# Optimization experiments

Measured on AMD Instinct MI355X. Metric: run time of the kernel, lower is better.

## Reference

```python
import jax, jax.numpy as jnp
import numpy as np

SEQ, BS, H, D = 2048, 2, 16, 64


def phi(x):
    # ELU(x / d**0.25) + 1
    return jax.nn.elu(x / (x.shape[-1] ** 0.25)) + 1.0


def setup_inputs() -> dict:
    key = jax.random.key(0)
    ks = jax.random.split(key, 5)
    return {
        "query_layer": jax.random.normal(ks[0], (SEQ, BS, H, D), jnp.float32),
        "key_layer": jax.random.normal(ks[1], (SEQ, BS, H, D), jnp.float32),
        "value_layer": jax.random.normal(ks[2], (SEQ, BS, H, D), jnp.float32),
        "attention_mask": jnp.zeros((BS, 1, SEQ, SEQ), dtype=bool),  # unused by forward
        "phi_k": jax.random.normal(ks[3], (1, H, D, 1), jnp.float32) / 10000.0,
        "phi_kv": jax.random.normal(ks[4], (1, H, D, D), jnp.float32) / 10000.0,
    }


def _ntk_attn(q, k, v, sum_phi_k, sum_phi_kv):
    # q,k,v: [bs,h,n,d]; sum_phi_k: [1,h,d,1]; sum_phi_kv: [1,h,d,d]
    d = q.shape[-1]
    nq, nk = q.shape[-2], k.shape[-2]
    kk = jnp.abs(sum_phi_k)
    Z = sum_phi_kv
    phi_q = phi(q)  # [bs,h,nq,d]
    A = jnp.einsum("bhqd,bhkd->bhqk", q, k) / jnp.sqrt(jnp.float32(d))
    max_A = jnp.max(A, axis=-1, keepdims=True)  # [bs,h,nq,1]
    exp_max_A = jnp.exp(max_A)
    A = jnp.exp(A - max_A)
    causal = jnp.tril(jnp.ones((nq, nk), jnp.float32), k=nk - nq)
    A = A * causal  # broadcast over [bs,h]
    D_norm = jnp.sum(A, axis=-1, keepdims=True) + jnp.matmul(phi_q, kk) / exp_max_A
    ctx = (jnp.matmul(A, v) + jnp.matmul(phi_q, Z) / exp_max_A) / D_norm
    return ctx  # [bs,h,nq,d]


def reference(query_layer, key_layer, value_layer, attention_mask, phi_k, phi_kv):
    # inputs are [seq, bs, h, d]; attention_mask is unused (module ignores it)
    q = jnp.transpose(query_layer, (1, 2, 0, 3)).astype(jnp.float32)
    k = jnp.transpose(key_layer, (1, 2, 0, 3)).astype(jnp.float32)
    v = jnp.transpose(value_layer, (1, 2, 0, 3)).astype(jnp.float32)
    ctx = _ntk_attn(q, k, v, phi_k, phi_kv)  # [bs,h,nq,d]
    ctx = jnp.transpose(ctx, (2, 0, 1, 3))  # [nq,bs,h,d]
    nq, bs, h, d = ctx.shape
    return ctx.reshape(nq, bs, h * d).astype(query_layer.dtype)
```

## Files before the change

### kernel.cpp

```cpp
#include <hip/hip_runtime.h>

#define SEQ 2048
#define BSZ 2
#define NHEAD 16
#define NBH (BSZ * NHEAD)
#define HDIM 64
#define QBLK 64
#define KVBLK 64
#define NQT (SEQ / QBLK)
#define ROWSTRIDE (BSZ * NHEAD * HDIM)

typedef __bf16 bf16x8 __attribute__((ext_vector_type(8)));
typedef __bf16 bf16x4 __attribute__((ext_vector_type(4)));
typedef float f32x4 __attribute__((ext_vector_type(4)));

#define AS1 __attribute__((address_space(1)))
#define AS3 __attribute__((address_space(3)))

__global__ __launch_bounds__(256)
void conv_all(const float* __restrict__ Kg, const float* __restrict__ Vg,
              const float* __restrict__ PKVg, __bf16* __restrict__ Kb,
              __bf16* __restrict__ Vt, __bf16* __restrict__ Ztb) {
  __shared__ __bf16 tt[HDIM][72];
  const int b = blockIdx.x;
  const int tid = threadIdx.x;

  if (b < 2048) {
    const int t = b * 256 + tid;
    const int s = t >> 8;
    const int bh = (t >> 3) & 31;
    const int d8 = (t & 7) * 8;
    const float* src = Kg + (size_t)s * ROWSTRIDE + bh * HDIM + d8;
    const float4 a = *(const float4*)src;
    const float4 bb = *(const float4*)(src + 4);
    bf16x8 o = {(__bf16)a.x, (__bf16)a.y, (__bf16)a.z, (__bf16)a.w,
                (__bf16)bb.x, (__bf16)bb.y, (__bf16)bb.z, (__bf16)bb.w};
    const int slot = (d8 >> 3) ^ (s & 7);
    *(bf16x8*)(Kb + ((size_t)bh * SEQ + s) * HDIM + slot * 8) = o;
  } else if (b < 3072) {
    const int t = b - 2048;
    const int kb = t & 31, bh = t >> 5;
    {
      const int r = tid >> 2, c16 = (tid & 3) * 16;
#pragma unroll
      for (int i = 0; i < 4; ++i) {
        const float4 v = *(const float4*)(Vg + (size_t)(kb * 64 + r) * ROWSTRIDE +
                                          bh * HDIM + c16 + 4 * i);
        tt[c16 + 4 * i + 0][r] = (__bf16)v.x;
        tt[c16 + 4 * i + 1][r] = (__bf16)v.y;
        tt[c16 + 4 * i + 2][r] = (__bf16)v.z;
        tt[c16 + 4 * i + 3][r] = (__bf16)v.w;
      }
    }
    __syncthreads();
    {
      const int d = tid >> 2, c2 = (tid & 3) * 2;
#pragma unroll
      for (int k8 = 0; k8 < 2; ++k8) {
        const int s8 = c2 + k8;
        const int pbase = (s8 ^ (d & 7)) * 8;
        __bf16 ov[8];
#pragma unroll
        for (int j = 0; j < 8; ++j) {
          const int p = pbase + j;
          const int P = p >> 5, g = (p >> 3) & 3, jj = p & 7;
          ov[j] = tt[d][32 * P + 16 * (jj >> 2) + 4 * g + (jj & 3)];
        }
        *(bf16x8*)(Vt + (((size_t)bh * 32 + kb) * 64 + d) * 64 + s8 * 8) =
            *(const bf16x8*)ov;
      }
    }
  } else {
    const int t = (b - 3072) * 256 + tid;
    const int lr = t & 15, lg = (t >> 4) & 3, c = (t >> 6) & 1;
    const int dj = (t >> 7) & 3, h = t >> 9;
    __bf16 o[8];
#pragma unroll
    for (int i = 0; i < 8; ++i)
      o[i] = (__bf16)PKVg[((size_t)h * 64 + 32 * c + 8 * lg + i) * 64 + dj * 16 + lr];
    *(bf16x8*)(Ztb + (size_t)t * 8) = *(const bf16x8*)o;
  }
}

__global__ __launch_bounds__(256, 4)
void ntk_attn(const float* __restrict__ Qg, const __bf16* __restrict__ Kb,
              const __bf16* __restrict__ Vt, const float* __restrict__ PKg,
              const __bf16* __restrict__ Ztb, float* __restrict__ Og) {
  __shared__ __bf16 Ks[2][KVBLK * HDIM];
  __shared__ __bf16 Vts[2][KVBLK * HDIM];

  const int tid = threadIdx.x;
  const int w = tid >> 6, l = tid & 63, lr = l & 15, lg = l >> 4;

  const int ord = blockIdx.x;
  const int bh = ord & 31, h = bh & (NHEAD - 1);
  const int v = ord >> 5;
  const int bx = (v < 16) ? v : 47 - v;
  const int q0 = bx * QBLK;
  const int ntile = bx + 1;
  const int headoff = bh * HDIM;
  const __bf16* Kbh = Kb + (size_t)bh * SEQ * HDIM;
  const __bf16* Vbh = Vt + (size_t)bh * SEQ * HDIM;

  auto stage = [&](int kb, int bb) {
    const char* gk = (const char*)Kbh + ((size_t)kb << 13) + (w << 11) + (l << 4);
    const char* gv = (const char*)Vbh + ((size_t)kb << 13) + (w << 11) + (l << 4);
    __bf16* lk = &Ks[bb][w << 10];
    __bf16* lv = &Vts[bb][w << 10];
    __builtin_amdgcn_global_load_lds((const AS1 unsigned*)gk,
                                     (AS3 unsigned*)lk, 16, 0, 0);
    __builtin_amdgcn_global_load_lds((const AS1 unsigned*)(gk + 1024),
                                     (AS3 unsigned*)(lk + 512), 16, 0, 0);
    __builtin_amdgcn_global_load_lds((const AS1 unsigned*)gv,
                                     (AS3 unsigned*)lv, 16, 0, 0);
    __builtin_amdgcn_global_load_lds((const AS1 unsigned*)(gv + 1024),
                                     (AS3 unsigned*)(lv + 512), 16, 0, 0);
  };

  stage(0, 0);

  bf16x8 aq[2], pq[2];
  {
    const float* qp = Qg + (size_t)(q0 + w * 16 + lr) * ROWSTRIDE + headoff + lg * 8;
#pragma unroll
    for (int c = 0; c < 2; ++c) {
      const float4 x0 = *(const float4*)(qp + 32 * c);
      const float4 x1 = *(const float4*)(qp + 32 * c + 4);
      const float f[8] = {x0.x, x0.y, x0.z, x0.w, x1.x, x1.y, x1.z, x1.w};
#pragma unroll
      for (int i = 0; i < 8; ++i) {
        aq[c][i] = (__bf16)(f[i] * 0.18033688011112042f);
        const float xs = f[i] * 0.3535533905932738f;
        pq[c][i] = (__bf16)(xs > 0.f ? xs + 1.f : __expf(xs));
      }
    }
  }

  const f32x4 z4 = {0.f, 0.f, 0.f, 0.f};
  f32x4 oacc[4] = {z4, z4, z4, z4};
  float lsum = 0.f;
  const int qa = q0 + w * 16 + lr;
  const int sw = lr & 7;

  __syncthreads();
  int cur = 0;

  for (int kb = 0; kb < ntile; ++kb) {
    const bool more = (kb + 1 < ntile);
    if (more) stage(kb + 1, cur ^ 1);

    bf16x8 kc[4][2];
#pragma unroll
    for (int nj = 0; nj < 4; ++nj)
#pragma unroll
      for (int c = 0; c < 2; ++c)
        kc[nj][c] = *(const bf16x8*)&Ks[cur][(nj * 16 + lr) * 64 +
                                            (((4 * c + lg) ^ sw) << 3)];
    bf16x8 vv[2][4];
#pragma unroll
    for (int P = 0; P < 2; ++P)
#pragma unroll
      for (int dj = 0; dj < 4; ++dj)
        vv[P][dj] = *(const bf16x8*)&Vts[cur][(dj * 16 + lr) * 64 +
                                             (((4 * P + lg) ^ sw) << 3)];

    f32x4 s4[4];
    __builtin_amdgcn_s_setprio(1);
#pragma unroll
    for (int nj = 0; nj < 4; ++nj) {
      f32x4 acc = z4;
#pragma unroll
      for (int c = 0; c < 2; ++c)
        acc = __builtin_amdgcn_mfma_f32_16x16x32_bf16(kc[nj][c], aq[c], acc, 0, 0, 0);
      s4[nj] = acc;
    }
    __builtin_amdgcn_s_setprio(0);

    bf16x4 p4[4];
    const bool diag = (kb == bx);
    const int kv0 = kb * KVBLK;
#pragma unroll
    for (int nj = 0; nj < 4; ++nj) {
#pragma unroll
      for (int r = 0; r < 4; ++r) {
        float e;
        if (diag) {
          const int kabs = kv0 + 16 * nj + 4 * lg + r;
          e = (kabs <= qa) ? __builtin_amdgcn_exp2f(s4[nj][r]) : 0.f;
        } else {
          e = __builtin_amdgcn_exp2f(s4[nj][r]);
        }
        lsum += e;
        p4[nj][r] = (__bf16)e;
      }
    }

    __builtin_amdgcn_s_setprio(1);
#pragma unroll
    for (int P = 0; P < 2; ++P) {
      const bf16x8 pa = __builtin_shufflevector(p4[2 * P], p4[2 * P + 1],
                                                0, 1, 2, 3, 4, 5, 6, 7);
#pragma unroll
      for (int dj = 0; dj < 4; ++dj)
        oacc[dj] = __builtin_amdgcn_mfma_f32_16x16x32_bf16(pa, vv[P][dj],
                                                           oacc[dj], 0, 0, 0);
    }
    __builtin_amdgcn_s_setprio(0);

    if (more) {
      __syncthreads();
      cur ^= 1;
    }
  }

  float den;
  {
    float pkk = 0.f;
#pragma unroll
    for (int c = 0; c < 2; ++c) {
      const float* kp = PKg + h * HDIM + 32 * c + 8 * lg;
      const float4 a = *(const float4*)kp;
      const float4 b = *(const float4*)(kp + 4);
      const float ka[8] = {a.x, a.y, a.z, a.w, b.x, b.y, b.z, b.w};
#pragma unroll
      for (int i = 0; i < 8; ++i)
        pkk += (float)pq[c][i] * fabsf(ka[i]);
    }
    pkk += __shfl_xor(pkk, 16);
    pkk += __shfl_xor(pkk, 32);
    float s = lsum;
    s += __shfl_xor(s, 16);
    s += __shfl_xor(s, 32);
    den = s + pkk;
  }

  f32x4 zacc[4] = {z4, z4, z4, z4};
  const __bf16* Zf = Ztb + (size_t)h * 4096;
  __builtin_amdgcn_s_setprio(1);
#pragma unroll
  for (int c = 0; c < 2; ++c) {
#pragma unroll
    for (int dj = 0; dj < 4; ++dj) {
      const bf16x8 bz = *(const bf16x8*)(Zf + ((dj * 2 + c) * 64 + l) * 8);
      zacc[dj] = __builtin_amdgcn_mfma_f32_16x16x32_bf16(pq[c], bz, zacc[dj], 0, 0, 0);
    }
  }
  __builtin_amdgcn_s_setprio(0);

#pragma unroll
  for (int r = 0; r < 4; ++r) {
    const float rd = 1.f / __shfl(den, lg * 4 + r);
    float* op = Og + (size_t)(q0 + w * 16 + lg * 4 + r) * ROWSTRIDE + headoff;
#pragma unroll
    for (int dj = 0; dj < 4; ++dj)
      op[dj * 16 + lr] = (oacc[dj][r] + zacc[dj][r]) * rd;
  }
}

extern "C" void kernel_launch(void* const* d_in, const int* in_sizes, int n_in,
                              void* d_out, int out_size, void* d_ws, size_t ws_size,
                              hipStream_t stream) {
  const float* Qg  = (const float*)d_in[0];
  const float* Kg  = (const float*)d_in[1];
  const float* Vg  = (const float*)d_in[2];
  const float* PKg  = (const float*)d_in[4];
  const float* PKVg = (const float*)d_in[5];
  float* Og = (float*)d_out;

  __bf16* Kb  = (__bf16*)d_ws;
  __bf16* Vt  = Kb + (size_t)NBH * SEQ * HDIM;
  __bf16* Ztb = Vt + (size_t)NBH * SEQ * HDIM;

  conv_all<<<dim3(2048 + 1024 + 32), dim3(256), 0, stream>>>(Kg, Vg, PKVg,
                                                             Kb, Vt, Ztb);
  ntk_attn<<<dim3(NQT * NBH), dim3(256), 0, stream>>>(Qg, Kb, Vt, PKg, Ztb, Og);
}
```

Baseline: 46.65 us.

## Process two 64-row query groups per block to reuse staged K/V tiles

```diff
diff --git a/kernel.cpp b/kernel.cpp
--- a/kernel.cpp
+++ b/kernel.cpp
@@ -5,7 +5,7 @@
 #define NHEAD 16
 #define NBH (BSZ * NHEAD)
 #define HDIM 64
-#define QBLK 64
+#define QBLK 128
 #define KVBLK 64
 #define NQT (SEQ / QBLK)
 #define ROWSTRIDE (BSZ * NHEAD * HDIM)
@@ -82,7 +82,7 @@
   }
 }
 
-__global__ __launch_bounds__(256, 4)
+__global__ __launch_bounds__(256, 2)
 void ntk_attn(const float* __restrict__ Qg, const __bf16* __restrict__ Kb,
               const __bf16* __restrict__ Vt, const float* __restrict__ PKg,
               const __bf16* __restrict__ Ztb, float* __restrict__ Og) {
@@ -95,9 +95,10 @@
   const int ord = blockIdx.x;
   const int bh = ord & 31, h = bh & (NHEAD - 1);
   const int v = ord >> 5;
-  const int bx = (v < 16) ? v : 47 - v;
+  const int bx = (v < 8) ? v : 23 - v;
   const int q0 = bx * QBLK;
-  const int ntile = bx + 1;
+  const int ntile = 2 * bx + 2;
+  const int dt0 = 2 * bx;
   const int headoff = bh * HDIM;
   const __bf16* Kbh = Kb + (size_t)bh * SEQ * HDIM;
   const __bf16* Vbh = Vt + (size_t)bh * SEQ * HDIM;
@@ -119,9 +120,11 @@
 
   stage(0, 0);
 
-  bf16x8 aq[2], pq[2];
-  {
-    const float* qp = Qg + (size_t)(q0 + w * 16 + lr) * ROWSTRIDE + headoff + lg * 8;
+  bf16x8 aq[2][2], pq[2][2];
+#pragma unroll
+  for (int g = 0; g < 2; ++g) {
+    const float* qp = Qg + (size_t)(q0 + 64 * g + w * 16 + lr) * ROWSTRIDE +
+                      headoff + lg * 8;
 #pragma unroll
     for (int c = 0; c < 2; ++c) {
       const float4 x0 = *(const float4*)(qp + 32 * c);
@@ -129,17 +132,19 @@
       const float f[8] = {x0.x, x0.y, x0.z, x0.w, x1.x, x1.y, x1.z, x1.w};
 #pragma unroll
       for (int i = 0; i < 8; ++i) {
-        aq[c][i] = (__bf16)(f[i] * 0.18033688011112042f);
+        aq[g][c][i] = (__bf16)(f[i] * 0.18033688011112042f);
         const float xs = f[i] * 0.3535533905932738f;
-        pq[c][i] = (__bf16)(xs > 0.f ? xs + 1.f : __expf(xs));
+        pq[g][c][i] = (__bf16)(xs > 0.f ? xs + 1.f : __expf(xs));
       }
     }
   }
 
   const f32x4 z4 = {0.f, 0.f, 0.f, 0.f};
-  f32x4 oacc[4] = {z4, z4, z4, z4};
-  float lsum = 0.f;
-  const int qa = q0 + w * 16 + lr;
+  f32x4 oacc[2][4] = {{z4, z4, z4, z4}, {z4, z4, z4, z4}};
+  float lsum[2] = {0.f, 0.f};
+  int qa[2];
+  qa[0] = q0 + w * 16 + lr;
+  qa[1] = q0 + 64 + w * 16 + lr;
   const int sw = lr & 7;
 
   __syncthreads();
@@ -164,48 +169,52 @@
         vv[P][dj] = *(const bf16x8*)&Vts[cur][(dj * 16 + lr) * 64 +
                                              (((4 * P + lg) ^ sw) << 3)];
 
-    f32x4 s4[4];
-    __builtin_amdgcn_s_setprio(1);
-#pragma unroll
-    for (int nj = 0; nj < 4; ++nj) {
-      f32x4 acc = z4;
-#pragma unroll
-      for (int c = 0; c < 2; ++c)
-        acc = __builtin_amdgcn_mfma_f32_16x16x32_bf16(kc[nj][c], aq[c], acc, 0, 0, 0);
-      s4[nj] = acc;
-    }
-    __builtin_amdgcn_s_setprio(0);
-
-    bf16x4 p4[4];
-    const bool diag = (kb == bx);
     const int kv0 = kb * KVBLK;
 #pragma unroll
-    for (int nj = 0; nj < 4; ++nj) {
-#pragma unroll
-      for (int r = 0; r < 4; ++r) {
-        float e;
-        if (diag) {
-          const int kabs = kv0 + 16 * nj + 4 * lg + r;
-          e = (kabs <= qa) ? __builtin_amdgcn_exp2f(s4[nj][r]) : 0.f;
-        } else {
-          e = __builtin_amdgcn_exp2f(s4[nj][r]);
+    for (int g = 0; g < 2; ++g) {
+      if (g == 0 && kb > dt0) continue;
+
+      f32x4 s4[4];
+      __builtin_amdgcn_s_setprio(1);
+#pragma unroll
+      for (int nj = 0; nj < 4; ++nj) {
+        f32x4 acc = z4;
+        acc = __builtin_amdgcn_mfma_f32_16x16x32_bf16(kc[nj][0], aq[g][0], acc, 0, 0, 0);
+        acc = __builtin_amdgcn_mfma_f32_16x16x32_bf16(kc[nj][1], aq[g][1], acc, 0, 0, 0);
+        s4[nj] = acc;
+      }
+      __builtin_amdgcn_s_setprio(0);
+
+      bf16x4 p4[4];
+      const bool diag = (kb == dt0 + g);
+#pragma unroll
+      for (int nj = 0; nj < 4; ++nj) {
+#pragma unroll
+        for (int r = 0; r < 4; ++r) {
+          float e;
+          if (diag) {
+            const int kabs = kv0 + 16 * nj + 4 * lg + r;
+            e = (kabs <= qa[g]) ? __builtin_amdgcn_exp2f(s4[nj][r]) : 0.f;
+          } else {
+            e = __builtin_amdgcn_exp2f(s4[nj][r]);
+          }
+          lsum[g] += e;
+          p4[nj][r] = (__bf16)e;
         }
-        lsum += e;
-        p4[nj][r] = (__bf16)e;
-      }
-    }
-
-    __builtin_amdgcn_s_setprio(1);
-#pragma unroll
-    for (int P = 0; P < 2; ++P) {
-      const bf16x8 pa = __builtin_shufflevector(p4[2 * P], p4[2 * P + 1],
-                                                0, 1, 2, 3, 4, 5, 6, 7);
-#pragma unroll
-      for (int dj = 0; dj < 4; ++dj)
-        oacc[dj] = __builtin_amdgcn_mfma_f32_16x16x32_bf16(pa, vv[P][dj],
-                                                           oacc[dj], 0, 0, 0);
-    }
-    __builtin_amdgcn_s_setprio(0);
+      }
+
+      __builtin_amdgcn_s_setprio(1);
+#pragma unroll
+      for (int P = 0; P < 2; ++P) {
+        const bf16x8 pa = __builtin_shufflevector(p4[2 * P], p4[2 * P + 1],
+                                                  0, 1, 2, 3, 4, 5, 6, 7);
+#pragma unroll
+        for (int dj = 0; dj < 4; ++dj)
+          oacc[g][dj] = __builtin_amdgcn_mfma_f32_16x16x32_bf16(pa, vv[P][dj],
+                                                                oacc[g][dj], 0, 0, 0);
+      }
+      __builtin_amdgcn_s_setprio(0);
+    }
 
     if (more) {
       __syncthreads();
@@ -213,47 +222,61 @@
     }
   }
 
-  float den;
+  float ka[16];
   {
-    float pkk = 0.f;
 #pragma unroll
     for (int c = 0; c < 2; ++c) {
       const float* kp = PKg + h * HDIM + 32 * c + 8 * lg;
       const float4 a = *(const float4*)kp;
       const float4 b = *(const float4*)(kp + 4);
-      const float ka[8] = {a.x, a.y, a.z, a.w, b.x, b.y, b.z, b.w};
+      ka[8 * c + 0] = fabsf(a.x); ka[8 * c + 1] = fabsf(a.y);
+      ka[8 * c + 2] = fabsf(a.z); ka[8 * c + 3] = fabsf(a.w);
+      ka[8 * c + 4] = fabsf(b.x); ka[8 * c + 5] = fabsf(b.y);
+      ka[8 * c + 6] = fabsf(b.z); ka[8 * c + 7] = fabsf(b.w);
+    }
+  }
+  bf16x8 bz[2][4];
+  const __bf16* Zf = Ztb + (size_t)h * 4096;
+#pragma unroll
+  for (int c = 0; c < 2; ++c)
+#pragma unroll
+    for (int dj = 0; dj < 4; ++dj)
+      bz[c][dj] = *(const bf16x8*)(Zf + ((dj * 2 + c) * 64 + l) * 8);
+
+#pragma unroll
+  for (int g = 0; g < 2; ++g) {
+    float pkk = 0.f;
+#pragma unroll
+    for (int c = 0; c < 2; ++c)
 #pragma unroll
       for (int i = 0; i < 8; ++i)
-        pkk += (float)pq[c][i] * fabsf(ka[i]);
-    }
+        pkk += (float)pq[g][c][i] * ka[8 * c + i];
     pkk += __shfl_xor(pkk, 16);
     pkk += __shfl_xor(pkk, 32);
-    float s = lsum;
+    float s = lsum[g];
     s += __shfl_xor(s, 16);
     s += __shfl_xor(s, 32);
-    den = s + pkk;
-  }
-
-  f32x4 zacc[4] = {z4, z4, z4, z4};
-  const __bf16* Zf = Ztb + (size_t)h * 4096;
-  __builtin_amdgcn_s_setprio(1);
-#pragma unroll
-  for (int c = 0; c < 2; ++c) {
-#pragma unroll
-    for (int dj = 0; dj < 4; ++dj) {
-      const bf16x8 bz = *(const bf16x8*)(Zf + ((dj * 2 + c) * 64 + l) * 8);
-      zacc[dj] = __builtin_amdgcn_mfma_f32_16x16x32_bf16(pq[c], bz, zacc[dj], 0, 0, 0);
-    }
-  }
-  __builtin_amdgcn_s_setprio(0);
-
-#pragma unroll
-  for (int r = 0; r < 4; ++r) {
-    const float rd = 1.f / __shfl(den, lg * 4 + r);
-    float* op = Og + (size_t)(q0 + w * 16 + lg * 4 + r) * ROWSTRIDE + headoff;
-#pragma unroll
-    for (int dj = 0; dj < 4; ++dj)
-      op[dj * 16 + lr] = (oacc[dj][r] + zacc[dj][r]) * rd;
+    const float den = s + pkk;
+
+    f32x4 zacc[4] = {z4, z4, z4, z4};
+    __builtin_amdgcn_s_setprio(1);
+#pragma unroll
+    for (int c = 0; c < 2; ++c)
+#pragma unroll
+      for (int dj = 0; dj < 4; ++dj)
+        zacc[dj] = __builtin_amdgcn_mfma_f32_16x16x32_bf16(pq[g][c], bz[c][dj],
+                                                           zacc[dj], 0, 0, 0);
+    __builtin_amdgcn_s_setprio(0);
+
+#pragma unroll
+    for (int r = 0; r < 4; ++r) {
+      const float rd = 1.f / __shfl(den, lg * 4 + r);
+      float* op = Og + (size_t)(q0 + 64 * g + w * 16 + lg * 4 + r) * ROWSTRIDE +
+                  headoff;
+#pragma unroll
+      for (int dj = 0; dj < 4; ++dj)
+        op[dj * 16 + lr] = (oacc[g][dj][r] + zacc[dj][r]) * rd;
+    }
   }
 }
 
```

Measured after the change: 46.48 us. About the same (-0.4%).

## Software-pipeline QK^T of next KV tile with PV of current tile

Applied to the files above, without the earlier changes.

```diff
diff --git a/kernel.cpp b/kernel.cpp
--- a/kernel.cpp
+++ b/kernel.cpp
@@ -142,20 +142,32 @@
   const int qa = q0 + w * 16 + lr;
   const int sw = lr & 7;
 
+  bf16x8 kc[4][2];
+  auto read_kc = [&](int bb) {
+#pragma unroll
+    for (int nj = 0; nj < 4; ++nj)
+#pragma unroll
+      for (int c = 0; c < 2; ++c)
+        kc[nj][c] = *(const bf16x8*)&Ks[bb][(nj * 16 + lr) * 64 +
+                                           (((4 * c + lg) ^ sw) << 3)];
+  };
+
+  f32x4 s4[4];
   __syncthreads();
+  read_kc(0);
+  __builtin_amdgcn_s_setprio(1);
+#pragma unroll
+  for (int nj = 0; nj < 4; ++nj) {
+    f32x4 acc = z4;
+    acc = __builtin_amdgcn_mfma_f32_16x16x32_bf16(kc[nj][0], aq[0], acc, 0, 0, 0);
+    acc = __builtin_amdgcn_mfma_f32_16x16x32_bf16(kc[nj][1], aq[1], acc, 0, 0, 0);
+    s4[nj] = acc;
+  }
+  __builtin_amdgcn_s_setprio(0);
+  if (ntile > 1) stage(1, 1);
+
   int cur = 0;
-
   for (int kb = 0; kb < ntile; ++kb) {
-    const bool more = (kb + 1 < ntile);
-    if (more) stage(kb + 1, cur ^ 1);
-
-    bf16x8 kc[4][2];
-#pragma unroll
-    for (int nj = 0; nj < 4; ++nj)
-#pragma unroll
-      for (int c = 0; c < 2; ++c)
-        kc[nj][c] = *(const bf16x8*)&Ks[cur][(nj * 16 + lr) * 64 +
-                                            (((4 * c + lg) ^ sw) << 3)];
     bf16x8 vv[2][4];
 #pragma unroll
     for (int P = 0; P < 2; ++P)
@@ -163,18 +175,6 @@
       for (int dj = 0; dj < 4; ++dj)
         vv[P][dj] = *(const bf16x8*)&Vts[cur][(dj * 16 + lr) * 64 +
                                              (((4 * P + lg) ^ sw) << 3)];
-
-    f32x4 s4[4];
-    __builtin_amdgcn_s_setprio(1);
-#pragma unroll
-    for (int nj = 0; nj < 4; ++nj) {
-      f32x4 acc = z4;
-#pragma unroll
-      for (int c = 0; c < 2; ++c)
-        acc = __builtin_amdgcn_mfma_f32_16x16x32_bf16(kc[nj][c], aq[c], acc, 0, 0, 0);
-      s4[nj] = acc;
-    }
-    __builtin_amdgcn_s_setprio(0);
 
     bf16x4 p4[4];
     const bool diag = (kb == bx);
@@ -195,21 +195,43 @@
       }
     }
 
-    __builtin_amdgcn_s_setprio(1);
-#pragma unroll
-    for (int P = 0; P < 2; ++P) {
-      const bf16x8 pa = __builtin_shufflevector(p4[2 * P], p4[2 * P + 1],
-                                                0, 1, 2, 3, 4, 5, 6, 7);
-#pragma unroll
-      for (int dj = 0; dj < 4; ++dj)
-        oacc[dj] = __builtin_amdgcn_mfma_f32_16x16x32_bf16(pa, vv[P][dj],
-                                                           oacc[dj], 0, 0, 0);
-    }
-    __builtin_amdgcn_s_setprio(0);
-
+    const bool more = (kb + 1 < ntile);
     if (more) {
       __syncthreads();
+      read_kc(cur ^ 1);
+      if (kb + 2 < ntile) stage(kb + 2, cur);
+
+      __builtin_amdgcn_s_setprio(1);
+#pragma unroll
+      for (int nj = 0; nj < 4; ++nj) {
+        f32x4 acc = z4;
+        acc = __builtin_amdgcn_mfma_f32_16x16x32_bf16(kc[nj][0], aq[0], acc, 0, 0, 0);
+        acc = __builtin_amdgcn_mfma_f32_16x16x32_bf16(kc[nj][1], aq[1], acc, 0, 0, 0);
+        s4[nj] = acc;
+      }
+#pragma unroll
+      for (int P = 0; P < 2; ++P) {
+        const bf16x8 pa = __builtin_shufflevector(p4[2 * P], p4[2 * P + 1],
+                                                  0, 1, 2, 3, 4, 5, 6, 7);
+#pragma unroll
+        for (int dj = 0; dj < 4; ++dj)
+          oacc[dj] = __builtin_amdgcn_mfma_f32_16x16x32_bf16(pa, vv[P][dj],
+                                                             oacc[dj], 0, 0, 0);
+      }
+      __builtin_amdgcn_s_setprio(0);
       cur ^= 1;
+    } else {
+      __builtin_amdgcn_s_setprio(1);
+#pragma unroll
+      for (int P = 0; P < 2; ++P) {
+        const bf16x8 pa = __builtin_shufflevector(p4[2 * P], p4[2 * P + 1],
+                                                  0, 1, 2, 3, 4, 5, 6, 7);
+#pragma unroll
+        for (int dj = 0; dj < 4; ++dj)
+          oacc[dj] = __builtin_amdgcn_mfma_f32_16x16x32_bf16(pa, vv[P][dj],
+                                                             oacc[dj], 0, 0, 0);
+      }
+      __builtin_amdgcn_s_setprio(0);
     }
   }
 
```

Result: slower. 63.77 us (+36.7%).
